# Performance work log

Hardware: AMD Instinct MI355X
Metric: run time of the kernel (lower is better)

Reference implementation:

```python
import jax, jax.numpy as jnp
import numpy as np
from functools import partial

B = 8192
BS = 6           # board_size
NSQ = BS * BS    # 36
FLAT = 128 * NSQ # 4608
EPS = 1e-5


def _conv(x, w, b):
    # x: (N,C,H,W), w: (O,I,3,3), SAME padding
    y = jax.lax.conv_general_dilated(x, w, (1, 1), 'SAME',
                                     dimension_numbers=('NCHW', 'OIHW', 'NCHW'))
    return y + b[None, :, None, None]


def _bn_eval(x, g, b, m, v):
    inv = jax.lax.rsqrt(v + EPS)
    return (x - m[None, :, None, None]) * (g * inv)[None, :, None, None] + b[None, :, None, None]


def _ln(x, g, b):
    mu = jnp.mean(x, axis=-1, keepdims=True)
    var = jnp.mean(jnp.square(x - mu), axis=-1, keepdims=True)
    return (x - mu) * jax.lax.rsqrt(var + EPS) * g + b


def _lin(x, w, b):
    return x @ w.T + b


def setup_inputs() -> dict:
    key = jax.random.key(0)
    ks = iter(jax.random.split(key, 64))
    nrm = lambda shape, s=0.05: jax.random.normal(next(ks), shape, jnp.float32) * s
    d = {}
    d['x'] = jax.random.normal(next(ks), (B, 4, BS, BS), jnp.float32)
    d['conv1_w'] = nrm((64, 4, 3, 3)); d['conv1_b'] = nrm((64,))
    d['bn1_g'] = jnp.ones((64,)); d['bn1_b'] = jnp.zeros((64,))
    d['bn1_m'] = nrm((64,)); d['bn1_v'] = jnp.ones((64,))
    d['conv2_w'] = nrm((128, 64, 3, 3)); d['conv2_b'] = nrm((128,))
    d['bn2_g'] = jnp.ones((128,)); d['bn2_b'] = jnp.zeros((128,))
    d['bn2_m'] = nrm((128,)); d['bn2_v'] = jnp.ones((128,))
    d['conv3_w'] = nrm((128, 128, 3, 3)); d['conv3_b'] = nrm((128,))
    d['bn3_g'] = jnp.ones((128,)); d['bn3_b'] = jnp.zeros((128,))
    d['bn3_m'] = nrm((128,)); d['bn3_v'] = jnp.ones((128,))
    d['pfc1_w'] = nrm((256, FLAT)); d['pfc1_b'] = nrm((256,))
    d['pln_g'] = jnp.ones((256,)); d['pln_b'] = jnp.zeros((256,))
    d['pfc2_w'] = nrm((NSQ, 256)); d['pfc2_b'] = nrm((NSQ,))
    d['mfc1_w'] = nrm((256, FLAT + NSQ)); d['mfc1_b'] = nrm((256,))
    d['mln_g'] = jnp.ones((256,)); d['mln_b'] = jnp.zeros((256,))
    d['mfc2_w'] = nrm((NSQ, 256)); d['mfc2_b'] = nrm((NSQ,))
    d['vfc1_w'] = nrm((256, FLAT)); d['vfc1_b'] = nrm((256,))
    d['vln_g'] = jnp.ones((256,)); d['vln_b'] = jnp.zeros((256,))
    d['vfc2_w'] = nrm((1, 256)); d['vfc2_b'] = nrm((1,))
    return d


def reference(x, conv1_w, conv1_b, bn1_g, bn1_b, bn1_m, bn1_v,
              conv2_w, conv2_b, bn2_g, bn2_b, bn2_m, bn2_v,
              conv3_w, conv3_b, bn3_g, bn3_b, bn3_m, bn3_v,
              pfc1_w, pfc1_b, pln_g, pln_b, pfc2_w, pfc2_b,
              mfc1_w, mfc1_b, mln_g, mln_b, mfc2_w, mfc2_b,
              vfc1_w, vfc1_b, vln_g, vln_b, vfc2_w, vfc2_b):
    h = jax.nn.relu(_bn_eval(_conv(x, conv1_w, conv1_b), bn1_g, bn1_b, bn1_m, bn1_v))
    h = jax.nn.relu(_bn_eval(_conv(h, conv2_w, conv2_b), bn2_g, bn2_b, bn2_m, bn2_v))
    h = jax.nn.relu(_bn_eval(_conv(h, conv3_w, conv3_b), bn3_g, bn3_b, bn3_m, bn3_v))
    feats = h.reshape(-1, FLAT)  # (B, 4608)

    piece_h = jax.nn.relu(_ln(_lin(feats, pfc1_w, pfc1_b), pln_g, pln_b))
    piece_logits = _lin(piece_h, pfc2_w, pfc2_b)  # (B, 36)

    # eval-mode: one-hot of argmax piece
    sel = jax.nn.one_hot(jnp.argmax(piece_logits, axis=1), NSQ, dtype=feats.dtype)
    move_in = jnp.concatenate([feats, sel], axis=1)  # (B, 4644)
    move_h = jax.nn.relu(_ln(_lin(move_in, mfc1_w, mfc1_b), mln_g, mln_b))
    move_logits = _lin(move_h, mfc2_w, mfc2_b)  # (B, 36)

    val_h = jax.nn.relu(_ln(_lin(feats, vfc1_w, vfc1_b), vln_g, vln_b))
    val = _lin(val_h, vfc2_w, vfc2_b)  # (B, 1)

    piece_adv = piece_logits - jnp.mean(piece_logits, axis=1, keepdims=True)
    move_adv = move_logits - jnp.mean(move_logits, axis=1, keepdims=True)

    # action_idx = i*36 + j  ->  fused outer-sum broadcast, reshape to (B, 1296)
    q = val[:, :, None] + piece_adv[:, :, None] + move_adv[:, None, :]
    return q.reshape(-1, NSQ * NSQ)
```

## Files before the change

### kernel.cpp

```cpp
#include <hip/hip_runtime.h>
#include <hip/hip_bf16.h>

#define BQ 8192
#define CHUNK 2048
#define NCHUNK 4
typedef __attribute__((ext_vector_type(8))) __bf16 bf16x8;
typedef __attribute__((ext_vector_type(4))) float f32x4;
typedef __attribute__((ext_vector_type(4))) int int4v;

__device__ __forceinline__ f32x4 mfma16(bf16x8 a, bf16x8 b, f32x4 c) {
    return __builtin_amdgcn_mfma_f32_16x16x32_bf16(a, b, c, 0, 0, 0);
}

__device__ __forceinline__ void split3(float v, __hip_bfloat16& s0,
                                       __hip_bfloat16& s1, __hip_bfloat16& s2) {
    s0 = __float2bfloat16(v);
    float r = v - __bfloat162float(s0);
    s1 = __float2bfloat16(r);
    r -= __bfloat162float(s1);
    s2 = __float2bfloat16(r);
}

__device__ __forceinline__ int pair_a(int pp) { return (0x211000 >> (4 * pp)) & 0xF; }
__device__ __forceinline__ int pair_w(int pp) { return (0x010210 >> (4 * pp)) & 0xF; }


__global__ void prep_scalars_k(
    const float* __restrict__ c1b, const float* __restrict__ g1,
    const float* __restrict__ b1,  const float* __restrict__ m1,
    const float* __restrict__ v1,
    const float* __restrict__ c2b, const float* __restrict__ g2,
    const float* __restrict__ b2,  const float* __restrict__ m2,
    const float* __restrict__ v2,
    const float* __restrict__ c3b, const float* __restrict__ g3,
    const float* __restrict__ b3,  const float* __restrict__ m3,
    const float* __restrict__ v3,
    const float* __restrict__ pfb, const float* __restrict__ vfb,
    const float* __restrict__ mfb,
    float* __restrict__ scale1, float* __restrict__ bias1f,
    float* __restrict__ scale2, float* __restrict__ bias2f,
    float* __restrict__ scale3, float* __restrict__ bias3f,
    float* __restrict__ biasfc)
{
    int t = threadIdx.x;
    if (t < 64) {
        float s = g1[t] * rsqrtf(v1[t] + 1e-5f);
        scale1[t] = s;
        bias1f[t] = (c1b[t] - m1[t]) * s + b1[t];
    }
    if (t < 128) {
        float s2 = g2[t] * rsqrtf(v2[t] + 1e-5f);
        scale2[t] = s2;
        bias2f[t] = (c2b[t] - m2[t]) * s2 + b2[t];
        float s3 = g3[t] * rsqrtf(v3[t] + 1e-5f);
        scale3[t] = s3;
        bias3f[t] = (c3b[t] - m3[t]) * s3 + b3[t];
    }
    if (t < 256)      biasfc[t] = pfb[t];
    else if (t < 512) biasfc[t] = vfb[t - 256];
    else              biasfc[t] = mfb[t - 512];
}

template<int CIN>
__global__ void prep_convw_k(const float* __restrict__ w,
                             __hip_bfloat16* __restrict__ wt, size_t planeW)
{
    int id = blockIdx.x * 256 + threadIdx.x;
    int kk = id & 31;
    int n  = (id >> 5) & 127;
    int kt = id >> 12;
    int k  = kt * 32 + kk;
    int s  = k / CIN;
    int i  = k & (CIN - 1);
    __hip_bfloat16 s0, s1, s2;
    split3(w[(n * CIN + i) * 9 + s], s0, s1, s2);
    size_t dest = (size_t)kt * 4096 + ((n >> 5) * 1024) + (((n >> 4) & 1) * 512)
                + ((kk >> 3) * 128) + ((n & 15) * 8) + (kk & 7);
    wt[dest] = s0; wt[dest + planeW] = s1; wt[dest + 2 * planeW] = s2;
}

__global__ void prep_bigw_k(const float* __restrict__ pw,
                            const float* __restrict__ vw,
                            const float* __restrict__ mw,
                            __hip_bfloat16* __restrict__ bigw, size_t planeBW)
{
    int id = blockIdx.x * 256 + threadIdx.x;
    int kk = id & 31;
    int n  = (id >> 5) % 768;
    int kt = id / (32 * 768);
    int k2 = kt * 32 + kk;
    int c  = k2 & 127, p = k2 >> 7;
    int k  = c * 36 + p;
    float v;
    if (n < 256)      v = pw[n * 4608 + k];
    else if (n < 512) v = vw[(n - 256) * 4608 + k];
    else              v = mw[(n - 512) * 4644 + k];
    __hip_bfloat16 s0, s1, s2;
    split3(v, s0, s1, s2);
    size_t dest = (size_t)kt * 24576 + ((n >> 7) * 4096) + (((n >> 6) & 1) * 2048)
                + (((n >> 4) & 3) * 512) + ((kk >> 3) * 128) + ((n & 15) * 8) + (kk & 7);
    bigw[dest] = s0; bigw[dest + planeBW] = s1; bigw[dest + 2 * planeBW] = s2;
}

__global__ void prep_selw_k(const float* __restrict__ mw,
                            float* __restrict__ selw)
{
    int j = blockIdx.x, d = threadIdx.x;
    selw[j * 256 + d] = mw[d * 4644 + 4608 + j];
}


__global__ __launch_bounds__(256)
void conv1_k(const float* __restrict__ x,
             const float* __restrict__ w,
             const float* __restrict__ scale, const float* __restrict__ biasf,
             __hip_bfloat16* __restrict__ out, size_t planeA,
             int b_base)
{
    __shared__ float wl[64 * 37];
    int tid = threadIdx.x;
    for (int c = tid; c < 64 * 36; c += 256) {
        int o = c / 36, k = c - o * 36;
        wl[o * 37 + k] = w[c];
    }
    __syncthreads();
    unsigned gid = blockIdx.x * 256 + tid;
    int o = gid & 63;
    unsigned bp = gid >> 6;
    unsigned b = bp / 36;
    int p = bp - b * 36;
    int py = p / 6, px = p - py * 6;
    const float* xb = x + (size_t)(b_base + b) * 4 * 36;
    float acc = 0.f;
#pragma unroll
    for (int i = 0; i < 4; ++i) {
#pragma unroll
        for (int s = 0; s < 9; ++s) {
            int ny = py + s / 3 - 1, nx = px + s % 3 - 1;
            if ((unsigned)ny < 6u && (unsigned)nx < 6u)
                acc += xb[i * 36 + ny * 6 + nx] * wl[o * 37 + i * 9 + s];
        }
    }
    float v = fmaxf(acc * scale[o] + biasf[o], 0.f);
    __hip_bfloat16 s0, s1, s2;
    split3(v, s0, s1, s2);
    size_t idx = (size_t)bp * 64 + o;
    out[idx] = s0; out[idx + planeA] = s1; out[idx + 2 * planeA] = s2;
}

template<int CIN>
__global__ __launch_bounds__(256, 4)
void conv_gemm_k(const __hip_bfloat16* __restrict__ in, size_t planeA,
                 const __hip_bfloat16* __restrict__ wt, size_t planeW,
                 const float* __restrict__ scale,
                 const float* __restrict__ biasf,
                 __hip_bfloat16* __restrict__ out, size_t planeO)
{
    constexpr int PS  = CIN + 8;
    constexpr int CPB = CIN / 32;
    constexpr int NSLICE = CPB * 9;
    constexpr int XS_ELEMS = 72 * PS;
    __shared__ __align__(16) __hip_bfloat16 smem[XS_ELEMS + CIN];
    __hip_bfloat16* xs = smem;

    const int tid  = threadIdx.x;
    const int wave = tid >> 6, lane = tid & 63;
    const int m16  = lane & 15, quad = lane >> 4;
    const int b0   = blockIdx.x * 2;

    if (tid < CIN) smem[XS_ELEMS + tid] = __float2bfloat16(0.f);

    f32x4 acc[5][2];
#pragma unroll
    for (int i = 0; i < 5; ++i) { acc[i][0] = f32x4{0,0,0,0}; acc[i][1] = f32x4{0,0,0,0}; }

    const int bo0 = wave * 1024 + lane * 8;
    const int bo1 = bo0 + 512;

    constexpr int CHPP = CIN / 8;
    for (int pp = 0; pp < 6; ++pp) {
        const __hip_bfloat16* inb = in + (size_t)pair_a(pp) * planeA + (size_t)b0 * 36 * CIN;
        const __hip_bfloat16* wP  = wt + (size_t)pair_w(pp) * planeW;
        const bool stage_x = (pp == 0) || (pair_a(pp) != pair_a(pp - 1));

        if (stage_x) {
            __syncthreads();
            for (int c = tid; c < 72 * CHPP; c += 256) {
                int pix = c / CHPP;
                int off = (c - pix * CHPP) * 8;
                *(int4v*)(xs + pix * PS + off) = *(const int4v*)(inb + pix * CIN + off);
            }
            __syncthreads();
        }

        bf16x8 wc0 = *(const bf16x8*)(wP + bo0);
        bf16x8 wc1 = *(const bf16x8*)(wP + bo1);

        for (int s = 0; s < 9; ++s) {
            const int dy = s / 3 - 1, dx = s % 3 - 1;
            int aoff[5];
#pragma unroll
            for (int rt = 0; rt < 5; ++rt) {
                int m   = rt * 16 + m16;
                int img = m >= 36;
                int p   = m - img * 36;
                int py  = p / 6, px = p - py * 6;
                int ny  = py + dy, nx = px + dx;
                bool ok = (m < 72) && ((unsigned)ny < 6u) && ((unsigned)nx < 6u);
                int base = ok ? ((img * 36 + ny * 6 + nx) * PS) : XS_ELEMS;
                aoff[rt] = base + quad * 8;
            }
#pragma unroll
            for (int c = 0; c < CPB; ++c) {
                const int kt = s * CPB + c;
                const int ktn = (kt + 1 < NSLICE) ? (kt + 1) : 0;
                const __hip_bfloat16* wN = wP + (size_t)ktn * 4096;
                bf16x8 wn0 = *(const bf16x8*)(wN + bo0);
                bf16x8 wn1 = *(const bf16x8*)(wN + bo1);
                const int coff = c * 32;
#pragma unroll
                for (int rt = 0; rt < 5; ++rt) {
                    bf16x8 af = *(const bf16x8*)(smem + aoff[rt] + coff);
                    acc[rt][0] = mfma16(af, wc0, acc[rt][0]);
                    acc[rt][1] = mfma16(af, wc1, acc[rt][1]);
                }
                wc0 = wn0; wc1 = wn1;
            }
        }
    }

#pragma unroll
    for (int ct = 0; ct < 2; ++ct) {
        const int n = wave * 32 + ct * 16 + m16;
        const float sc = scale[n], bi = biasf[n];
#pragma unroll
        for (int rt = 0; rt < 5; ++rt) {
            const int mrow = rt * 16 + quad * 4;
            if (mrow < 72) {
#pragma unroll
                for (int r = 0; r < 4; ++r) {
                    float v = fmaxf(acc[rt][ct][r] * sc + bi, 0.f);
                    __hip_bfloat16 s0, s1, s2;
                    split3(v, s0, s1, s2);
                    size_t idx = (size_t)(b0 * 36 + mrow + r) * 128 + n;
                    out[idx] = s0; out[idx + planeO] = s1; out[idx + 2 * planeO] = s2;
                }
            }
        }
    }
}


__global__ __launch_bounds__(256, 3)
void fc_partial_k(const __hip_bfloat16* __restrict__ A, size_t planeF,
                  const __hip_bfloat16* __restrict__ Bw, size_t planeBW,
                  float* __restrict__ partial)
{
    constexpr int ABUF = 4096;
    __shared__ __align__(16) __hip_bfloat16 smem[2 * ABUF];
    const int tid = threadIdx.x, wave = tid >> 6, lane = tid & 63;
    const int m16 = lane & 15, quad = lane >> 4;
    const int mblk = blockIdx.x & 15;
    int rest = blockIdx.x >> 4;
    const int nblk = rest % 6;
    rest /= 6;
    const int pp = rest % 6;
    const int ks = rest / 6;
    const int kt0 = ks * 72, ktend = kt0 + 72;
    const size_t m0 = (size_t)mblk * 128;
    const int wr = wave >> 1, wc = wave & 1;

    const __hip_bfloat16* Ap = A + (size_t)pair_a(pp) * planeF;
    const __hip_bfloat16* Bp = Bw + (size_t)pair_w(pp) * planeBW + (size_t)nblk * 4096;

    f32x4 acc[4][4];
#pragma unroll
    for (int i = 0; i < 4; ++i)
#pragma unroll
        for (int j = 0; j < 4; ++j) acc[i][j] = f32x4{0,0,0,0};

    const int cr = tid >> 2, co = (tid & 3) * 8;
    int ao[4];
#pragma unroll
    for (int i = 0; i < 4; ++i) ao[i] = wr * 2048 + i * 512 + lane * 8;
    const int bofs = wc * 2048 + lane * 8;
    const int adst = ((cr >> 4) & 3) * 512 + (tid & 3) * 128 + (cr & 15) * 8;

    auto ldA = [&](int kt, int4v& a0, int4v& a1) {
        const __hip_bfloat16* base = Ap + (m0 + cr) * 4608 + kt * 32 + co;
        a0 = *(const int4v*)base;
        a1 = *(const int4v*)(base + (size_t)64 * 4608);
    };
    auto ldB = [&](int kt, bf16x8* bf) {
        const __hip_bfloat16* base = Bp + (size_t)kt * 24576 + bofs;
#pragma unroll
        for (int i = 0; i < 4; ++i) bf[i] = *(const bf16x8*)(base + i * 512);
    };
    auto stA = [&](int buf, int4v a0, int4v a1) {
        __hip_bfloat16* base = smem + buf * ABUF;
        *(int4v*)(base + adst) = a0;
        *(int4v*)(base + 2048 + adst) = a1;
    };

    int4v pa, pb, qa, qb;
    bf16x8 bfc[4], bf1[4];
    {
        int4v a0, a1;
        ldA(kt0, a0, a1);
        ldB(kt0, bfc);
        ldA(kt0 + 1, pa, pb);
        ldB(kt0 + 1, bf1);
        stA(0, a0, a1);
    }
    __syncthreads();
    int cur = 0;

#pragma unroll 2
    for (int kt = kt0; kt < ktend; ++kt) {
        const int ktn = (kt + 2 < ktend) ? (kt + 2) : kt0;
        bf16x8 bfn[4];
        ldA(ktn, qa, qb);
        ldB(ktn, bfn);
        const __hip_bfloat16* base = smem + cur * ABUF;
        bf16x8 af[4];
#pragma unroll
        for (int i = 0; i < 4; ++i) af[i] = *(const bf16x8*)(base + ao[i]);
#pragma unroll
        for (int i = 0; i < 4; ++i)
#pragma unroll
            for (int j = 0; j < 4; ++j)
                acc[i][j] = mfma16(af[i], bfc[j], acc[i][j]);
        if (kt + 1 < ktend) stA(cur ^ 1, pa, pb);
        __syncthreads();
        cur ^= 1;
        pa = qa; pb = qb;
#pragma unroll
        for (int i = 0; i < 4; ++i) bfc[i] = bf1[i];
#pragma unroll
        for (int i = 0; i < 4; ++i) bf1[i] = bfn[i];
    }

    float* outp = partial + (size_t)rest * CHUNK * 768;
    const int n0 = nblk * 128;
#pragma unroll
    for (int i = 0; i < 4; ++i) {
        const int row = wr * 64 + i * 16 + quad * 4;
#pragma unroll
        for (int j = 0; j < 4; ++j) {
            const int col = n0 + wc * 64 + j * 16 + m16;
#pragma unroll
            for (int r = 0; r < 4; ++r)
                outp[(m0 + row + r) * 768 + col] = acc[i][j][r];
        }
    }
}


__global__ __launch_bounds__(256)
void heads_k(const float* __restrict__ partial,
             const float* __restrict__ biasfc,
             const float* __restrict__ pln_g, const float* __restrict__ pln_b,
             const float* __restrict__ pfc2_w, const float* __restrict__ pfc2_b,
             const float* __restrict__ mln_g, const float* __restrict__ mln_b,
             const float* __restrict__ mfc2_w, const float* __restrict__ mfc2_b,
             const float* __restrict__ vln_g, const float* __restrict__ vln_b,
             const float* __restrict__ vfc2_w, const float* __restrict__ vfc2_b,
             const float* __restrict__ selw,
             float* __restrict__ q,
             int b_base)
{
    __shared__ float hp[256], hv[256], hm[256];
    __shared__ float pl[36], ml[36];
    __shared__ float red[4];
    __shared__ float valv, plm_s, mlm_s;
    __shared__ int amax_s;

    const int tid = threadIdx.x, wave = tid >> 6, lane = tid & 63;
    const size_t b = blockIdx.x;
    const size_t bg = b_base + b;

    float pp = biasfc[tid], vv = biasfc[256 + tid], mm = biasfc[512 + tid];
#pragma unroll
    for (int k = 0; k < 12; ++k) {
        const float* row = partial + (size_t)k * CHUNK * 768 + b * 768;
        pp += row[tid]; vv += row[256 + tid]; mm += row[512 + tid];
    }

    auto warpSum = [&](float v) {
        v += __shfl_xor(v, 1);  v += __shfl_xor(v, 2);  v += __shfl_xor(v, 4);
        v += __shfl_xor(v, 8);  v += __shfl_xor(v, 16); v += __shfl_xor(v, 32);
        return v;
    };
    auto blockSum = [&](float v) {
        v = warpSum(v);
        if (lane == 0) red[wave] = v;
        __syncthreads();
        float s = red[0] + red[1] + red[2] + red[3];
        __syncthreads();
        return s;
    };
    auto lnrelu = [&](float x, const float* g, const float* bb) {
        float mu  = blockSum(x) * (1.f / 256.f);
        float d   = x - mu;
        float var = blockSum(d * d) * (1.f / 256.f);
        float y   = d * rsqrtf(var + 1e-5f) * g[tid] + bb[tid];
        return fmaxf(y, 0.f);
    };

    hp[tid] = lnrelu(pp, pln_g, pln_b);
    hv[tid] = lnrelu(vv, vln_g, vln_b);
    __syncthreads();

    {
        float h0 = hp[lane], h1 = hp[64 + lane], h2 = hp[128 + lane], h3 = hp[192 + lane];
#pragma unroll
        for (int jj = 0; jj < 9; ++jj) {
            int j = wave * 9 + jj;
            const float* wr_ = pfc2_w + j * 256;
            float s = h0 * wr_[lane] + h1 * wr_[64 + lane]
                    + h2 * wr_[128 + lane] + h3 * wr_[192 + lane];
            s = warpSum(s);
            if (lane == 0) pl[j] = s + pfc2_b[j];
        }
        if (wave == 0) {
            float g0 = hv[lane], g1 = hv[64 + lane], g2 = hv[128 + lane], g3 = hv[192 + lane];
            float s = g0 * vfc2_w[lane] + g1 * vfc2_w[64 + lane]
                    + g2 * vfc2_w[128 + lane] + g3 * vfc2_w[192 + lane];
            s = warpSum(s);
            if (lane == 0) valv = s + vfc2_b[0];
        }
    }
    __syncthreads();
    if (tid == 0) {
        float m = -1e30f, s = 0.f; int idx = 0;
        for (int j = 0; j < 36; ++j) { float v = pl[j]; s += v; if (v > m) { m = v; idx = j; } }
        plm_s = s * (1.f / 36.f); amax_s = idx;
    }
    __syncthreads();

    mm += selw[amax_s * 256 + tid];
    hm[tid] = lnrelu(mm, mln_g, mln_b);
    __syncthreads();
    {
        float h0 = hm[lane], h1 = hm[64 + lane], h2 = hm[128 + lane], h3 = hm[192 + lane];
#pragma unroll
        for (int jj = 0; jj < 9; ++jj) {
            int j = wave * 9 + jj;
            const float* wr_ = mfc2_w + j * 256;
            float s = h0 * wr_[lane] + h1 * wr_[64 + lane]
                    + h2 * wr_[128 + lane] + h3 * wr_[192 + lane];
            s = warpSum(s);
            if (lane == 0) ml[j] = s + mfc2_b[j];
        }
    }
    __syncthreads();
    if (tid == 0) {
        float s = 0.f;
        for (int j = 0; j < 36; ++j) s += ml[j];
        mlm_s = s * (1.f / 36.f);
    }
    __syncthreads();

    const float val = valv, plm = plm_s, mlm = mlm_s;
    for (int idx = tid; idx < 1296; idx += 256) {
        int i = idx / 36, j = idx - i * 36;
        q[bg * 1296 + idx] = val + (pl[i] - plm) + (ml[j] - mlm);
    }
}


extern "C" void kernel_launch(void* const* d_in, const int* in_sizes, int n_in,
                              void* d_out, int out_size, void* d_ws, size_t ws_size,
                              hipStream_t stream)
{
    const float* x       = (const float*)d_in[0];
    const float* conv1_w = (const float*)d_in[1];
    const float* conv1_b = (const float*)d_in[2];
    const float* bn1_g   = (const float*)d_in[3];
    const float* bn1_b   = (const float*)d_in[4];
    const float* bn1_m   = (const float*)d_in[5];
    const float* bn1_v   = (const float*)d_in[6];
    const float* conv2_w = (const float*)d_in[7];
    const float* conv2_b = (const float*)d_in[8];
    const float* bn2_g   = (const float*)d_in[9];
    const float* bn2_b   = (const float*)d_in[10];
    const float* bn2_m   = (const float*)d_in[11];
    const float* bn2_v   = (const float*)d_in[12];
    const float* conv3_w = (const float*)d_in[13];
    const float* conv3_b = (const float*)d_in[14];
    const float* bn3_g   = (const float*)d_in[15];
    const float* bn3_b   = (const float*)d_in[16];
    const float* bn3_m   = (const float*)d_in[17];
    const float* bn3_v   = (const float*)d_in[18];
    const float* pfc1_w  = (const float*)d_in[19];
    const float* pfc1_b  = (const float*)d_in[20];
    const float* pln_g   = (const float*)d_in[21];
    const float* pln_b   = (const float*)d_in[22];
    const float* pfc2_w  = (const float*)d_in[23];
    const float* pfc2_b  = (const float*)d_in[24];
    const float* mfc1_w  = (const float*)d_in[25];
    const float* mfc1_b  = (const float*)d_in[26];
    const float* mln_g   = (const float*)d_in[27];
    const float* mln_b   = (const float*)d_in[28];
    const float* mfc2_w  = (const float*)d_in[29];
    const float* mfc2_b  = (const float*)d_in[30];
    const float* vfc1_w  = (const float*)d_in[31];
    const float* vfc1_b  = (const float*)d_in[32];
    const float* vln_g   = (const float*)d_in[33];
    const float* vln_b   = (const float*)d_in[34];
    const float* vfc2_w  = (const float*)d_in[35];
    const float* vfc2_b  = (const float*)d_in[36];

    const size_t planeW2 = 576 * 128;
    const size_t planeW3 = 1152 * 128;
    const size_t planeBW = (size_t)4608 * 768;
    const size_t planeA1 = (size_t)CHUNK * 36 * 64;
    const size_t planeA2 = (size_t)CHUNK * 36 * 128;

    char* ws = (char*)d_ws;
    size_t off = 0;
    auto alloc = [&](size_t bytes) -> char* {
        char* p = ws + off; off += (bytes + 255) & ~(size_t)255; return p;
    };
    __hip_bfloat16* w2t  = (__hip_bfloat16*)alloc(3 * planeW2 * 2);
    __hip_bfloat16* w3t  = (__hip_bfloat16*)alloc(3 * planeW3 * 2);
    __hip_bfloat16* bigw = (__hip_bfloat16*)alloc(3 * planeBW * 2);
    float* selw   = (float*)alloc(36 * 256 * 4);
    float* scale1 = (float*)alloc(64 * 4);
    float* bias1f = (float*)alloc(64 * 4);
    float* scale2 = (float*)alloc(128 * 4);
    float* bias2f = (float*)alloc(128 * 4);
    float* scale3 = (float*)alloc(128 * 4);
    float* bias3f = (float*)alloc(128 * 4);
    float* biasfc = (float*)alloc(768 * 4);
    char* A1 = alloc(3 * planeA2 * 2);
    char* A2 = alloc((size_t)12 * CHUNK * 768 * 4);

    prep_scalars_k<<<1, 768, 0, stream>>>(
        conv1_b, bn1_g, bn1_b, bn1_m, bn1_v,
        conv2_b, bn2_g, bn2_b, bn2_m, bn2_v,
        conv3_b, bn3_g, bn3_b, bn3_m, bn3_v,
        pfc1_b, vfc1_b, mfc1_b,
        scale1, bias1f, scale2, bias2f, scale3, bias3f, biasfc);
    prep_convw_k<64><<<288, 256, 0, stream>>>(conv2_w, w2t, planeW2);
    prep_convw_k<128><<<576, 256, 0, stream>>>(conv3_w, w3t, planeW3);
    prep_bigw_k<<<13824, 256, 0, stream>>>(pfc1_w, vfc1_w, mfc1_w, bigw, planeBW);
    prep_selw_k<<<36, 256, 0, stream>>>(mfc1_w, selw);

    __hip_bfloat16* h1s  = (__hip_bfloat16*)A1;
    __hip_bfloat16* h2s  = (__hip_bfloat16*)A2;
    __hip_bfloat16* h3s  = (__hip_bfloat16*)A1;
    float*          fpar = (float*)A2;

    for (int cchunk = 0; cchunk < NCHUNK; ++cchunk) {
        const int b_base = cchunk * CHUNK;
        conv1_k<<<CHUNK * 36 * 64 / 256, 256, 0, stream>>>(
            x, conv1_w, scale1, bias1f, h1s, planeA1, b_base);
        conv_gemm_k<64><<<CHUNK / 2, 256, 0, stream>>>(
            h1s, planeA1, w2t, planeW2, scale2, bias2f, h2s, planeA2);
        conv_gemm_k<128><<<CHUNK / 2, 256, 0, stream>>>(
            h2s, planeA2, w3t, planeW3, scale3, bias3f, h3s, planeA2);
        fc_partial_k<<<1152, 256, 0, stream>>>(h3s, planeA2, bigw, planeBW, fpar);
        heads_k<<<CHUNK, 256, 0, stream>>>(fpar, biasfc,
            pln_g, pln_b, pfc2_w, pfc2_b,
            mln_g, mln_b, mfc2_w, mfc2_b,
            vln_g, vln_b, vfc2_w, vfc2_b,
            selw, (float*)d_out, b_base);
    }
}
```

Baseline: 1.763 ms.

## Reuse A tiles across multiple weight split planes in FC partial GEMM

The split-precision FC GEMM previously launched one block per (A-plane, W-plane) pair, so each A tile was reloaded for every pair that used it. Now each block takes one A plane and runs it against several weight planes (3, 2 or 1) over a shorter K range. Each staged A tile in shared memory feeds several MFMA passes, which cuts global A traffic and syncs per MFMA. The cost is unequal work per block (slot types differ in K length and weight count), a changed partial-slot layout that the reduction must match, and more register pressure from the extra B buffers.

After: 1.698 ms. 1.04x faster.

```diff
diff --git a/kernel.cpp b/kernel.cpp
--- a/kernel.cpp
+++ b/kernel.cpp
@@ -251,6 +251,101 @@
 }
 
 
+template<int NW, int NKT>
+__device__ __forceinline__ void fc_body(
+    const __hip_bfloat16* __restrict__ Ap,
+    const __hip_bfloat16* __restrict__ Bp,
+    size_t planeBW, int kt0,
+    float* __restrict__ outp, size_t m0,
+    __hip_bfloat16* smem, int tid, int wave, int lane)
+{
+    constexpr int ABUF = 4096;
+    constexpr int NPH = NW * NKT;
+    const int m16 = lane & 15, quad = lane >> 4;
+    const int wr = wave >> 1, wc = wave & 1;
+    const int cr = tid >> 2, co = (tid & 3) * 8;
+
+    f32x4 acc[4][4];
+#pragma unroll
+    for (int i = 0; i < 4; ++i)
+#pragma unroll
+        for (int j = 0; j < 4; ++j) acc[i][j] = f32x4{0,0,0,0};
+
+    int ao[4];
+#pragma unroll
+    for (int i = 0; i < 4; ++i) ao[i] = wr * 2048 + i * 512 + lane * 8;
+    const int bofs = wc * 2048 + lane * 8;
+    const int adst = ((cr >> 4) & 3) * 512 + (tid & 3) * 128 + (cr & 15) * 8;
+
+    auto ldA = [&](int ktr, int4v& a0, int4v& a1) {
+        const __hip_bfloat16* base = Ap + (m0 + cr) * 4608 + (kt0 + ktr) * 32 + co;
+        a0 = *(const int4v*)base;
+        a1 = *(const int4v*)(base + (size_t)64 * 4608);
+    };
+    auto ldB = [&](int p, bf16x8* bf) {
+        const int ktr = p / NW, w = p - ktr * NW;
+        const __hip_bfloat16* base = Bp + (size_t)w * planeBW
+                                   + (size_t)(kt0 + ktr) * 24576 + bofs;
+#pragma unroll
+        for (int i = 0; i < 4; ++i) bf[i] = *(const bf16x8*)(base + i * 512);
+    };
+    auto stA = [&](int buf, int4v a0, int4v a1) {
+        __hip_bfloat16* base = smem + buf * ABUF;
+        *(int4v*)(base + adst) = a0;
+        *(int4v*)(base + 2048 + adst) = a1;
+    };
+
+    int4v pa0, pa1, qa0, qa1;
+    bf16x8 Bc[4], B1[4], Bn[4];
+    {
+        int4v a0, a1;
+        ldA(0, a0, a1);
+        ldB(0, Bc);
+        ldA(1, pa0, pa1);
+        if (NPH > 1) ldB(1, B1);
+        stA(0, a0, a1);
+    }
+    __syncthreads();
+    int cur = 0;
+
+    for (int ktr = 0; ktr < NKT; ++ktr) {
+        { int ktn = (ktr + 2 < NKT) ? (ktr + 2) : 0; ldA(ktn, qa0, qa1); }
+        const __hip_bfloat16* base = smem + cur * ABUF;
+        bf16x8 af[4];
+#pragma unroll
+        for (int i = 0; i < 4; ++i) af[i] = *(const bf16x8*)(base + ao[i]);
+#pragma unroll
+        for (int w = 0; w < NW; ++w) {
+            int p2 = ktr * NW + w + 2;
+            if (p2 >= NPH) p2 = 0;
+            ldB(p2, Bn);
+#pragma unroll
+            for (int i = 0; i < 4; ++i)
+#pragma unroll
+                for (int j = 0; j < 4; ++j)
+                    acc[i][j] = mfma16(af[i], Bc[j], acc[i][j]);
+#pragma unroll
+            for (int i = 0; i < 4; ++i) { Bc[i] = B1[i]; B1[i] = Bn[i]; }
+        }
+        if (ktr + 1 < NKT) stA(cur ^ 1, pa0, pa1);
+        __syncthreads();
+        cur ^= 1;
+        pa0 = qa0; pa1 = qa1;
+    }
+
+#pragma unroll
+    for (int i = 0; i < 4; ++i) {
+        const int row = wr * 64 + i * 16 + quad * 4;
+#pragma unroll
+        for (int j = 0; j < 4; ++j) {
+            const int col = wc * 64 + j * 16 + m16;
+#pragma unroll
+            for (int r = 0; r < 4; ++r)
+                outp[(m0 + row + r) * 768 + col] = acc[i][j][r];
+        }
+    }
+}
+
 __global__ __launch_bounds__(256, 3)
 void fc_partial_k(const __hip_bfloat16* __restrict__ A, size_t planeF,
                   const __hip_bfloat16* __restrict__ Bw, size_t planeBW,
@@ -259,99 +354,21 @@
     constexpr int ABUF = 4096;
     __shared__ __align__(16) __hip_bfloat16 smem[2 * ABUF];
     const int tid = threadIdx.x, wave = tid >> 6, lane = tid & 63;
-    const int m16 = lane & 15, quad = lane >> 4;
     const int mblk = blockIdx.x & 15;
     int rest = blockIdx.x >> 4;
     const int nblk = rest % 6;
-    rest /= 6;
-    const int pp = rest % 6;
-    const int ks = rest / 6;
-    const int kt0 = ks * 72, ktend = kt0 + 72;
+    const int slot = rest / 6;
     const size_t m0 = (size_t)mblk * 128;
-    const int wr = wave >> 1, wc = wave & 1;
-
-    const __hip_bfloat16* Ap = A + (size_t)pair_a(pp) * planeF;
-    const __hip_bfloat16* Bp = Bw + (size_t)pair_w(pp) * planeBW + (size_t)nblk * 4096;
-
-    f32x4 acc[4][4];
-#pragma unroll
-    for (int i = 0; i < 4; ++i)
-#pragma unroll
-        for (int j = 0; j < 4; ++j) acc[i][j] = f32x4{0,0,0,0};
-
-    const int cr = tid >> 2, co = (tid & 3) * 8;
-    int ao[4];
-#pragma unroll
-    for (int i = 0; i < 4; ++i) ao[i] = wr * 2048 + i * 512 + lane * 8;
-    const int bofs = wc * 2048 + lane * 8;
-    const int adst = ((cr >> 4) & 3) * 512 + (tid & 3) * 128 + (cr & 15) * 8;
-
-    auto ldA = [&](int kt, int4v& a0, int4v& a1) {
-        const __hip_bfloat16* base = Ap + (m0 + cr) * 4608 + kt * 32 + co;
-        a0 = *(const int4v*)base;
-        a1 = *(const int4v*)(base + (size_t)64 * 4608);
-    };
-    auto ldB = [&](int kt, bf16x8* bf) {
-        const __hip_bfloat16* base = Bp + (size_t)kt * 24576 + bofs;
-#pragma unroll
-        for (int i = 0; i < 4; ++i) bf[i] = *(const bf16x8*)(base + i * 512);
-    };
-    auto stA = [&](int buf, int4v a0, int4v a1) {
-        __hip_bfloat16* base = smem + buf * ABUF;
-        *(int4v*)(base + adst) = a0;
-        *(int4v*)(base + 2048 + adst) = a1;
-    };
-
-    int4v pa, pb, qa, qb;
-    bf16x8 bfc[4], bf1[4];
-    {
-        int4v a0, a1;
-        ldA(kt0, a0, a1);
-        ldB(kt0, bfc);
-        ldA(kt0 + 1, pa, pb);
-        ldB(kt0 + 1, bf1);
-        stA(0, a0, a1);
-    }
-    __syncthreads();
-    int cur = 0;
-
-#pragma unroll 2
-    for (int kt = kt0; kt < ktend; ++kt) {
-        const int ktn = (kt + 2 < ktend) ? (kt + 2) : kt0;
-        bf16x8 bfn[4];
-        ldA(ktn, qa, qb);
-        ldB(ktn, bfn);
-        const __hip_bfloat16* base = smem + cur * ABUF;
-        bf16x8 af[4];
-#pragma unroll
-        for (int i = 0; i < 4; ++i) af[i] = *(const bf16x8*)(base + ao[i]);
-#pragma unroll
-        for (int i = 0; i < 4; ++i)
-#pragma unroll
-            for (int j = 0; j < 4; ++j)
-                acc[i][j] = mfma16(af[i], bfc[j], acc[i][j]);
-        if (kt + 1 < ktend) stA(cur ^ 1, pa, pb);
-        __syncthreads();
-        cur ^= 1;
-        pa = qa; pb = qb;
-#pragma unroll
-        for (int i = 0; i < 4; ++i) bfc[i] = bf1[i];
-#pragma unroll
-        for (int i = 0; i < 4; ++i) bf1[i] = bfn[i];
-    }
-
-    float* outp = partial + (size_t)rest * CHUNK * 768;
-    const int n0 = nblk * 128;
-#pragma unroll
-    for (int i = 0; i < 4; ++i) {
-        const int row = wr * 64 + i * 16 + quad * 4;
-#pragma unroll
-        for (int j = 0; j < 4; ++j) {
-            const int col = n0 + wc * 64 + j * 16 + m16;
-#pragma unroll
-            for (int r = 0; r < 4; ++r)
-                outp[(m0 + row + r) * 768 + col] = acc[i][j][r];
-        }
+
+    const __hip_bfloat16* Bp = Bw + (size_t)nblk * 4096;
+    float* outp = partial + (size_t)slot * CHUNK * 768 + (size_t)nblk * 128;
+
+    if (slot < 6) {
+        fc_body<3, 24>(A, Bp, planeBW, slot * 24, outp, m0, smem, tid, wave, lane);
+    } else if (slot < 10) {
+        fc_body<2, 36>(A + planeF, Bp, planeBW, (slot - 6) * 36, outp, m0, smem, tid, wave, lane);
+    } else {
+        fc_body<1, 72>(A + 2 * planeF, Bp, planeBW, (slot - 10) * 72, outp, m0, smem, tid, wave, lane);
     }
 }
 
```
